# Optimization experiments

Hardware: AMD Instinct MI355X
Metric: run time of the kernel (lower is better)

## Reference

```python
import jax, jax.numpy as jnp
import numpy as np

N = 50000      # nodes
E = 800000     # edges
F_IN = 128     # input features
H = 128        # hidden width
C = 64         # classes


def _glorot(key, fan_in, fan_out):
    lim = float(np.sqrt(6.0 / (fan_in + fan_out)))
    return jax.random.uniform(key, (fan_in, fan_out), jnp.float32, -lim, lim)


def setup_inputs() -> dict:
    key = jax.random.key(0)
    ks = jax.random.split(key, 8)
    x = jax.random.normal(ks[0], (N, F_IN), jnp.float32)
    edge_index = jax.random.randint(ks[1], (2, E), 0, N, dtype=jnp.int64)
    return {
        "x": x,
        "edge_index": edge_index,
        "W0": _glorot(ks[2], F_IN, H), "b0": jnp.zeros((H,), jnp.float32),
        "W1": _glorot(ks[3], H, H),    "b1": jnp.zeros((H,), jnp.float32),
        "W2": _glorot(ks[4], H, C),    "b2": jnp.zeros((C,), jnp.float32),
    }


def _gcn_norm(edge_index, n):
    # add self-loops, then symmetric normalization D^-1/2 A D^-1/2
    loop = jnp.arange(n, dtype=edge_index.dtype)
    src = jnp.concatenate([edge_index[0], loop])   # message source j
    dst = jnp.concatenate([edge_index[1], loop])   # aggregation target i
    deg = jax.ops.segment_sum(jnp.ones_like(dst, jnp.float32), dst, num_segments=n)
    dinv = jnp.where(deg > 0, jax.lax.rsqrt(jnp.maximum(deg, 1.0)), 0.0)
    norm = dinv[src] * dinv[dst]                   # [E+N]
    return src, dst, norm


def _gcn_conv(x, W, b, src, dst, norm, n):
    h = x @ W                                      # [N, out]
    msg = norm[:, None] * h[src]                   # gather [E+N, out]
    out = jax.ops.segment_sum(msg, dst, num_segments=n)  # scatter-add
    return out + b


def reference(x, edge_index, W0, b0, W1, b1, W2, b2):
    n = x.shape[0]
    src, dst, norm = _gcn_norm(edge_index, n)
    h = _gcn_conv(x, W0, b0, src, dst, norm, n)
    h = h * jax.nn.sigmoid(h)                      # swish
    h = _gcn_conv(h, W1, b1, src, dst, norm, n)
    h = h * jax.nn.sigmoid(h)
    h = _gcn_conv(h, W2, b2, src, dst, norm, n)
    return jax.nn.log_softmax(h, axis=1)
```

## Files before the change

kernel.cpp:

```cpp
#include <hip/hip_runtime.h>


#define NODES_PER_BUCKET 1024
#define MAX_BUCKETS 64
#define CVT_BLOCKS 160

typedef __attribute__((ext_vector_type(8))) short short8;
typedef __attribute__((ext_vector_type(4))) float f32x4;

__device__ inline unsigned bf16_rn(float x) {
    unsigned u = __float_as_uint(x);
    return (u + 0x7fffu + ((u >> 16) & 1u)) >> 16;
}
__device__ inline float bf_lo(unsigned u) { return __uint_as_float(u << 16); }
__device__ inline float bf_hi(unsigned u) { return __uint_as_float(u & 0xffff0000u); }

__global__ __launch_bounds__(256) void prep_k(const int* __restrict__ dst, int e,
                                              int* __restrict__ bcnt,
                                              const float* __restrict__ W0,
                                              const float* __restrict__ W1,
                                              const float* __restrict__ W2,
                                              unsigned short* __restrict__ Wt) {
    const int t = threadIdx.x;
    if (blockIdx.x < CVT_BLOCKS) {
        int id = blockIdx.x * 256 + t;
        const float* W;
        int out, loc;
        if (id < 16384)      { W = W0; out = 128; loc = id; }
        else if (id < 32768) { W = W1; out = 128; loc = id - 16384; }
        else                 { W = W2; out = 64;  loc = id - 32768; }
        int o = loc >> 7, k = loc & 127;
        Wt[id] = (unsigned short)bf16_rn(W[k * out + o]);
        return;
    }
    __shared__ int h[MAX_BUCKETS];
    if (t < MAX_BUCKETS) h[t] = 0;
    __syncthreads();
    const int i0 = (blockIdx.x - CVT_BLOCKS) * 4096;
#pragma unroll
    for (int k = 0; k < 16; ++k) {
        int i = i0 + t + k * 256;
        if (i < e) atomicAdd(&h[dst[i] >> 10], 1);
    }
    __syncthreads();
    if (t < MAX_BUCKETS && h[t]) atomicAdd(&bcnt[t], h[t]);
}

__global__ __launch_bounds__(512) void scatter_k(const int* __restrict__ src,
                                                 const int* __restrict__ dst,
                                                 int e,
                                                 const int* __restrict__ bcnt,
                                                 int* __restrict__ scur,
                                                 unsigned* __restrict__ pairs) {
    __shared__ int bbase_s[MAX_BUCKETS];
    __shared__ int cnt[MAX_BUCKETS];
    __shared__ int cur[MAX_BUCKETS];
    __shared__ int gb[MAX_BUCKETS];
    const int t = threadIdx.x;
    if (t < MAX_BUCKETS) {
        int v = bcnt[t];
        int x = v;
#pragma unroll
        for (int off = 1; off < 64; off <<= 1) {
            int y = __shfl_up(x, off);
            if ((t & 63) >= off) x += y;
        }
        bbase_s[t] = x - v;
        cnt[t] = 0;
    }
    __syncthreads();
    const int i0 = blockIdx.x * 8192;
    int d[16];
#pragma unroll
    for (int k = 0; k < 16; ++k) {
        int i = i0 + t + k * 512;
        d[k] = (i < e) ? dst[i] : -1;
        if (d[k] >= 0) atomicAdd(&cnt[d[k] >> 10], 1);
    }
    __syncthreads();
    if (t < MAX_BUCKETS) {
        gb[t] = cnt[t] ? bbase_s[t] + atomicAdd(&scur[t], cnt[t]) : 0;
        cur[t] = 0;
    }
    __syncthreads();
#pragma unroll
    for (int k = 0; k < 16; ++k) {
        int i = i0 + t + k * 512;
        if (d[k] >= 0) {
            int b = d[k] >> 10;
            int r = atomicAdd(&cur[b], 1);
            pairs[gb[b] + r] = ((unsigned)src[i] << 10) | ((unsigned)d[k] & 1023u);
        }
    }
}

__global__ __launch_bounds__(1024) void build_k(const unsigned* __restrict__ pairs,
                                                const int* __restrict__ bcnt,
                                                int n, int e,
                                                int* __restrict__ rp,
                                                float* __restrict__ dinv,
                                                int* __restrict__ col) {
    __shared__ int hist[1024];
    __shared__ int tsum[1024];
    __shared__ int sE[2];
    const int t = threadIdx.x;
    if (t < MAX_BUCKETS) {
        int v = bcnt[t];
        int x = v;
#pragma unroll
        for (int off = 1; off < 64; off <<= 1) {
            int y = __shfl_up(x, off);
            if ((t & 63) >= off) x += y;
        }
        if (t == blockIdx.x) { sE[0] = x - v; sE[1] = x; }
    }
    hist[t] = 0;
    __syncthreads();
    const int ebase = sE[0];
    const int eend = sE[1];
    for (int i = ebase + t; i < eend; i += 1024)
        atomicAdd(&hist[pairs[i] & 1023u], 1);
    __syncthreads();
    const int deg = hist[t];
    tsum[t] = deg;
    __syncthreads();
    for (int off = 1; off < 1024; off <<= 1) {
        int x = (t >= off) ? tsum[t - off] : 0;
        __syncthreads();
        tsum[t] += x;
        __syncthreads();
    }
    const int excl = tsum[t] - deg;
    const int node0 = blockIdx.x << 10;
    if (node0 + t < n) {
        rp[node0 + t] = ebase + excl;
        dinv[node0 + t] = rsqrtf((float)(deg + 1));
    }
    hist[t] = excl;
    __syncthreads();
    for (int i = ebase + t; i < eend; i += 1024) {
        unsigned p = pairs[i];
        int r = atomicAdd(&hist[p & 1023u], 1);
        col[ebase + r] = (int)(p >> 10);
    }
    if (blockIdx.x == 0 && t == 0) rp[n] = e;
}

__global__ __launch_bounds__(256) void mfma_gemm0_k(
    const float* __restrict__ Af,
    const unsigned short* __restrict__ Wt,
    const float* __restrict__ dinv,
    unsigned short* __restrict__ G,
    int n) {
    __shared__ unsigned short lds[256 * 128];
    unsigned short* As = lds;
    unsigned short* Ws = lds + 128 * 128;

    const int tid = threadIdx.x;
    const int row0 = blockIdx.x * 128;

#pragma unroll
    for (int p = 0; p < 8; ++p) {
        int id = p * 256 + tid;
        int r = id >> 4, c = id & 15;
        uint4 v = make_uint4(0, 0, 0, 0);
        if (row0 + r < n) {
            const float4* fp = (const float4*)&Af[(size_t)(row0 + r) * 128 + c * 8];
            float4 v0 = fp[0], v1 = fp[1];
            v.x = bf16_rn(v0.x) | (bf16_rn(v0.y) << 16);
            v.y = bf16_rn(v0.z) | (bf16_rn(v0.w) << 16);
            v.z = bf16_rn(v1.x) | (bf16_rn(v1.y) << 16);
            v.w = bf16_rn(v1.z) | (bf16_rn(v1.w) << 16);
        }
        int bo = r * 256 + ((c * 16) ^ ((r & 7) << 4));
        *(uint4*)((char*)As + bo) = v;
    }
#pragma unroll
    for (int p = 0; p < 8; ++p) {
        int id = p * 256 + tid;
        int r = id >> 4, c = id & 15;
        uint4 v = *(const uint4*)&Wt[(size_t)r * 128 + c * 8];
        int bo = r * 256 + ((c * 16) ^ ((r & 7) << 4));
        *(uint4*)((char*)Ws + bo) = v;
    }
    __syncthreads();

    const int wid = tid >> 6, lane = tid & 63;
    const int lq = lane >> 4, lr = lane & 15;
    const int woff = wid * 32;

    f32x4 acc[2][8] = {};
#pragma unroll
    for (int ks = 0; ks < 4; ++ks) {
        short8 a[2];
#pragma unroll
        for (int m = 0; m < 2; ++m) {
            int r = woff + m * 16 + lr;
            int bo = r * 256 + ((lq * 16 + ks * 64) ^ ((r & 7) << 4));
            a[m] = *(const short8*)((const char*)As + bo);
        }
#pragma unroll
        for (int nf = 0; nf < 8; ++nf) {
            int c = nf * 16 + lr;
            int bo = c * 256 + ((lq * 16 + ks * 64) ^ ((c & 7) << 4));
            short8 b = *(const short8*)((const char*)Ws + bo);
            acc[0][nf] = __builtin_amdgcn_mfma_f32_16x16x32_bf16(a[0], b, acc[0][nf], 0, 0, 0);
            acc[1][nf] = __builtin_amdgcn_mfma_f32_16x16x32_bf16(a[1], b, acc[1][nf], 0, 0, 0);
        }
    }

#pragma unroll
    for (int m = 0; m < 2; ++m) {
#pragma unroll
        for (int j = 0; j < 4; ++j) {
            int r = row0 + woff + m * 16 + lq * 4 + j;
            if (r < n) {
                float d = dinv[r];
#pragma unroll
                for (int nf = 0; nf < 8; ++nf)
                    G[(size_t)r * 128 + nf * 16 + lr] =
                        (unsigned short)bf16_rn(d * acc[m][nf][j]);
            }
        }
    }
}

__device__ inline void acc8(float* a, uint4 u) {
    a[0] += bf_lo(u.x); a[1] += bf_hi(u.x);
    a[2] += bf_lo(u.y); a[3] += bf_hi(u.y);
    a[4] += bf_lo(u.z); a[5] += bf_hi(u.z);
    a[6] += bf_lo(u.w); a[7] += bf_hi(u.w);
}

template <int OUT>
__global__ __launch_bounds__(256, 4) void agg_gemm_k(
    const uint4* __restrict__ G4,
    const int* __restrict__ rp,
    const int* __restrict__ col,
    const float* __restrict__ dinv,
    const float* __restrict__ bias,
    const unsigned short* __restrict__ Wt,
    unsigned short* __restrict__ Gn,
    int n) {
    constexpr int NF = OUT / 16;
    __shared__ unsigned short lds[(64 + OUT) * 128];
    unsigned short* As = lds;
    unsigned short* Ws = lds + 64 * 128;

    const int tid = threadIdx.x;
    const int base = blockIdx.x * 64;
    const int sl = tid & 15;

    const float4 bl = *(const float4*)&bias[sl * 8];
    const float4 bh = *(const float4*)&bias[sl * 8 + 4];
#pragma unroll
    for (int q = 0; q < 4; ++q) {
        const int local = (tid >> 4) + q * 16;
        const int i = base + local;
        uint4 o = make_uint4(0, 0, 0, 0);
        if (i < n) {
            float a[8] = {0.f, 0.f, 0.f, 0.f, 0.f, 0.f, 0.f, 0.f};
            acc8(a, G4[(size_t)i * 16 + sl]);
            const int s = rp[i], e = rp[i + 1];
            int p = s;
            for (; p + 8 <= e; p += 8) {
                uint4 v[8];
#pragma unroll
                for (int k = 0; k < 8; ++k) {
                    int j = col[p + k];
                    v[k] = G4[(size_t)j * 16 + sl];
                }
#pragma unroll
                for (int k = 0; k < 8; ++k) acc8(a, v[k]);
            }
            if (p < e) {
                const int m = e - p;
                uint4 v[8];
#pragma unroll
                for (int k = 0; k < 8; ++k) {
                    int j = col[min(p + k, e - 1)];
                    v[k] = G4[(size_t)j * 16 + sl];
                }
#pragma unroll
                for (int k = 0; k < 8; ++k)
                    if (k < m) acc8(a, v[k]);
            }
            const float d = dinv[i];
            float r[8];
            r[0] = d * a[0] + bl.x; r[1] = d * a[1] + bl.y;
            r[2] = d * a[2] + bl.z; r[3] = d * a[3] + bl.w;
            r[4] = d * a[4] + bh.x; r[5] = d * a[5] + bh.y;
            r[6] = d * a[6] + bh.z; r[7] = d * a[7] + bh.w;
#pragma unroll
            for (int k = 0; k < 8; ++k) r[k] = r[k] / (1.f + expf(-r[k]));
            o.x = bf16_rn(r[0]) | (bf16_rn(r[1]) << 16);
            o.y = bf16_rn(r[2]) | (bf16_rn(r[3]) << 16);
            o.z = bf16_rn(r[4]) | (bf16_rn(r[5]) << 16);
            o.w = bf16_rn(r[6]) | (bf16_rn(r[7]) << 16);
        }
        int bo = local * 256 + ((sl * 16) ^ ((local & 7) << 4));
        *(uint4*)((char*)As + bo) = o;
    }

#pragma unroll
    for (int p = 0; p < OUT / 16; ++p) {
        int id = p * 256 + tid;
        int r = id >> 4, c = id & 15;
        uint4 v = *(const uint4*)&Wt[(size_t)r * 128 + c * 8];
        int bo = r * 256 + ((c * 16) ^ ((r & 7) << 4));
        *(uint4*)((char*)Ws + bo) = v;
    }
    __syncthreads();

    const int wid = tid >> 6, lane = tid & 63;
    const int lq = lane >> 4, lr = lane & 15;
    const int woff = wid * 16;

    f32x4 acc[NF] = {};
#pragma unroll
    for (int ks = 0; ks < 4; ++ks) {
        int r = woff + lr;
        int bo = r * 256 + ((lq * 16 + ks * 64) ^ ((r & 7) << 4));
        short8 a = *(const short8*)((const char*)As + bo);
#pragma unroll
        for (int nf = 0; nf < NF; ++nf) {
            int c = nf * 16 + lr;
            int wo = c * 256 + ((lq * 16 + ks * 64) ^ ((c & 7) << 4));
            short8 b = *(const short8*)((const char*)Ws + wo);
            acc[nf] = __builtin_amdgcn_mfma_f32_16x16x32_bf16(a, b, acc[nf], 0, 0, 0);
        }
    }

#pragma unroll
    for (int j = 0; j < 4; ++j) {
        int r = base + woff + lq * 4 + j;
        if (r < n) {
            float d = dinv[r];
#pragma unroll
            for (int nf = 0; nf < NF; ++nf)
                Gn[(size_t)r * OUT + nf * 16 + lr] =
                    (unsigned short)bf16_rn(d * acc[nf][j]);
        }
    }
}

__global__ __launch_bounds__(512, 4) void agg_lsm_k(const uint2* __restrict__ G2,
                                                    const int* __restrict__ rp,
                                                    const int* __restrict__ col,
                                                    const float* __restrict__ dinv,
                                                    const float* __restrict__ bias,
                                                    float* __restrict__ out, int n) {
    const int i = (blockIdx.x * blockDim.x + threadIdx.x) >> 4;
    const int sl = threadIdx.x & 15;
    if (i >= n) return;

    float a[4] = {0.f, 0.f, 0.f, 0.f};
    {
        uint2 u = G2[(size_t)i * 16 + sl];
        a[0] += bf_lo(u.x); a[1] += bf_hi(u.x);
        a[2] += bf_lo(u.y); a[3] += bf_hi(u.y);
    }
    const int s = rp[i], e = rp[i + 1];
    int p = s;
    for (; p + 8 <= e; p += 8) {
        uint2 v[8];
#pragma unroll
        for (int k = 0; k < 8; ++k) {
            int j = col[p + k];
            v[k] = G2[(size_t)j * 16 + sl];
        }
#pragma unroll
        for (int k = 0; k < 8; ++k) {
            a[0] += bf_lo(v[k].x); a[1] += bf_hi(v[k].x);
            a[2] += bf_lo(v[k].y); a[3] += bf_hi(v[k].y);
        }
    }
    if (p < e) {
        const int m = e - p;
        uint2 v[8];
#pragma unroll
        for (int k = 0; k < 8; ++k) {
            int j = col[min(p + k, e - 1)];
            v[k] = G2[(size_t)j * 16 + sl];
        }
#pragma unroll
        for (int k = 0; k < 8; ++k)
            if (k < m) {
                a[0] += bf_lo(v[k].x); a[1] += bf_hi(v[k].x);
                a[2] += bf_lo(v[k].y); a[3] += bf_hi(v[k].y);
            }
    }

    const float d = dinv[i];
    const float4 bv = *(const float4*)&bias[sl * 4];
    float lg[4];
    lg[0] = d * a[0] + bv.x; lg[1] = d * a[1] + bv.y;
    lg[2] = d * a[2] + bv.z; lg[3] = d * a[3] + bv.w;

    float m0 = fmaxf(fmaxf(lg[0], lg[1]), fmaxf(lg[2], lg[3]));
#pragma unroll
    for (int off = 1; off < 16; off <<= 1) m0 = fmaxf(m0, __shfl_xor(m0, off));
    float es = expf(lg[0] - m0) + expf(lg[1] - m0) +
               expf(lg[2] - m0) + expf(lg[3] - m0);
#pragma unroll
    for (int off = 1; off < 16; off <<= 1) es += __shfl_xor(es, off);
    const float lse = m0 + logf(es);
    float4 o;
    o.x = lg[0] - lse; o.y = lg[1] - lse; o.z = lg[2] - lse; o.w = lg[3] - lse;
    *(float4*)&out[(size_t)i * 64 + sl * 4] = o;
}

extern "C" void kernel_launch(void* const* d_in, const int* in_sizes, int n_in,
                              void* d_out, int out_size, void* d_ws, size_t ws_size,
                              hipStream_t stream) {
    const float* x = (const float*)d_in[0];
    const int* ei = (const int*)d_in[1];
    const float* W0 = (const float*)d_in[2];
    const float* b0 = (const float*)d_in[3];
    const float* W1 = (const float*)d_in[4];
    const float* b1 = (const float*)d_in[5];
    const float* W2 = (const float*)d_in[6];
    const float* b2 = (const float*)d_in[7];
    float* out = (float*)d_out;

    const int n = in_sizes[0] / 128;
    const int e = in_sizes[1] / 2;
    const int* src = ei;
    const int* dst = ei + e;

    char* ws = (char*)d_ws;
    size_t off = 0;
    auto alloc = [&](size_t bytes) -> void* {
        void* p = ws + off;
        off += (bytes + 255) & ~(size_t)255;
        return p;
    };
    int* bcnt = (int*)alloc(MAX_BUCKETS * 4 * 2);
    int* scur = bcnt + MAX_BUCKETS;
    int* rp = (int*)alloc((size_t)(n + 1) * 4);
    float* dinv = (float*)alloc((size_t)n * 4);
    int* col = (int*)alloc((size_t)e * 4);
    unsigned* pairs = (unsigned*)alloc((size_t)e * 4);
    unsigned short* wt = (unsigned short*)alloc(40960 * 2);
    unsigned short* ga = (unsigned short*)alloc((size_t)n * 256);
    unsigned short* gb = (unsigned short*)alloc((size_t)n * 256);

    unsigned short* w0t = wt;
    unsigned short* w1t = wt + 16384;
    unsigned short* w2t = wt + 32768;

    hipMemsetAsync(bcnt, 0, MAX_BUCKETS * 4 * 2, stream);
    prep_k<<<CVT_BLOCKS + (e + 4095) / 4096, 256, 0, stream>>>(dst, e, bcnt,
                                                               W0, W1, W2, wt);
    scatter_k<<<(e + 8191) / 8192, 512, 0, stream>>>(src, dst, e, bcnt, scur, pairs);
    const int nbuck = (n + NODES_PER_BUCKET - 1) / NODES_PER_BUCKET;
    build_k<<<nbuck, 1024, 0, stream>>>(pairs, bcnt, n, e, rp, dinv, col);

    const int gb128 = (n + 127) / 128;
    const int fb = (n + 63) / 64;
    const int ab = (n + 31) / 32;

    mfma_gemm0_k<<<gb128, 256, 0, stream>>>(x, w0t, dinv, ga, n);
    agg_gemm_k<128><<<fb, 256, 0, stream>>>((const uint4*)ga, rp, col, dinv, b0,
                                            w1t, gb, n);
    agg_gemm_k<64><<<fb, 256, 0, stream>>>((const uint4*)gb, rp, col, dinv, b1,
                                           w2t, ga, n);
    agg_lsm_k<<<ab, 512, 0, stream>>>((const uint2*)ga, rp, col, dinv, b2, out, n);
}
```

Before: 162.5 us.

## Shrink fused agg-GEMM tile to 32 rows and read weights directly from global

The fused aggregation+GEMM kernel now handles 32 nodes per block instead of 64. The four waves are split into two row strips times two output-column halves. The weight tile is no longer staged in LDS; each wave loads its B fragments straight from global memory, where the weights should stay cache-resident. This cuts LDS use and per-block staging cost, raising occupancy and block count for the latency-bound gather. In exchange, each block re-reads weights from global/L2, and there are twice as many blocks.

```diff
diff --git a/kernel.cpp b/kernel.cpp
--- a/kernel.cpp
+++ b/kernel.cpp
@@ -242,19 +242,18 @@
     const unsigned short* __restrict__ Wt,
     unsigned short* __restrict__ Gn,
     int n) {
-    constexpr int NF = OUT / 16;
-    __shared__ unsigned short lds[(64 + OUT) * 128];
-    unsigned short* As = lds;
-    unsigned short* Ws = lds + 64 * 128;
+    constexpr int HC = OUT / 2;
+    constexpr int NF = OUT / 32;
+    __shared__ unsigned short As[32 * 128];
 
     const int tid = threadIdx.x;
-    const int base = blockIdx.x * 64;
+    const int base = blockIdx.x * 32;
     const int sl = tid & 15;
 
     const float4 bl = *(const float4*)&bias[sl * 8];
     const float4 bh = *(const float4*)&bias[sl * 8 + 4];
 #pragma unroll
-    for (int q = 0; q < 4; ++q) {
+    for (int q = 0; q < 2; ++q) {
         const int local = (tid >> 4) + q * 16;
         const int i = base + local;
         uint4 o = make_uint4(0, 0, 0, 0);
@@ -301,44 +300,35 @@
         int bo = local * 256 + ((sl * 16) ^ ((local & 7) << 4));
         *(uint4*)((char*)As + bo) = o;
     }
-
-#pragma unroll
-    for (int p = 0; p < OUT / 16; ++p) {
-        int id = p * 256 + tid;
-        int r = id >> 4, c = id & 15;
-        uint4 v = *(const uint4*)&Wt[(size_t)r * 128 + c * 8];
-        int bo = r * 256 + ((c * 16) ^ ((r & 7) << 4));
-        *(uint4*)((char*)Ws + bo) = v;
-    }
     __syncthreads();
 
     const int wid = tid >> 6, lane = tid & 63;
     const int lq = lane >> 4, lr = lane & 15;
-    const int woff = wid * 16;
+    const int strip = wid >> 1;
+    const int half = wid & 1;
 
     f32x4 acc[NF] = {};
 #pragma unroll
     for (int ks = 0; ks < 4; ++ks) {
-        int r = woff + lr;
+        int r = strip * 16 + lr;
         int bo = r * 256 + ((lq * 16 + ks * 64) ^ ((r & 7) << 4));
         short8 a = *(const short8*)((const char*)As + bo);
 #pragma unroll
         for (int nf = 0; nf < NF; ++nf) {
-            int c = nf * 16 + lr;
-            int wo = c * 256 + ((lq * 16 + ks * 64) ^ ((c & 7) << 4));
-            short8 b = *(const short8*)((const char*)Ws + wo);
+            int c = half * HC + nf * 16 + lr;
+            short8 b = *(const short8*)&Wt[(size_t)c * 128 + ks * 32 + lq * 8];
             acc[nf] = __builtin_amdgcn_mfma_f32_16x16x32_bf16(a, b, acc[nf], 0, 0, 0);
         }
     }
 
 #pragma unroll
     for (int j = 0; j < 4; ++j) {
-        int r = base + woff + lq * 4 + j;
+        int r = base + strip * 16 + lq * 4 + j;
         if (r < n) {
             float d = dinv[r];
 #pragma unroll
             for (int nf = 0; nf < NF; ++nf)
-                Gn[(size_t)r * OUT + nf * 16 + lr] =
+                Gn[(size_t)r * OUT + half * HC + nf * 16 + lr] =
                     (unsigned short)bf16_rn(d * acc[nf][j]);
         }
     }
@@ -443,7 +433,7 @@
     unsigned* pairs = (unsigned*)alloc((size_t)e * 4);
     unsigned short* wt = (unsigned short*)alloc(40960 * 2);
     unsigned short* ga = (unsigned short*)alloc((size_t)n * 256);
-    unsigned short* gb = (unsigned short*)alloc((size_t)n * 256);
+    unsigned short* gbuf = (unsigned short*)alloc((size_t)n * 256);
 
     unsigned short* w0t = wt;
     unsigned short* w1t = wt + 16384;
@@ -457,13 +447,13 @@
     build_k<<<nbuck, 1024, 0, stream>>>(pairs, bcnt, n, e, rp, dinv, col);
 
     const int gb128 = (n + 127) / 128;
-    const int fb = (n + 63) / 64;
+    const int fb = (n + 31) / 32;
     const int ab = (n + 31) / 32;
 
     mfma_gemm0_k<<<gb128, 256, 0, stream>>>(x, w0t, dinv, ga, n);
     agg_gemm_k<128><<<fb, 256, 0, stream>>>((const uint4*)ga, rp, col, dinv, b0,
-                                            w1t, gb, n);
-    agg_gemm_k<64><<<fb, 256, 0, stream>>>((const uint4*)gb, rp, col, dinv, b1,
+                                            w1t, gbuf, n);
+    agg_gemm_k<64><<<fb, 256, 0, stream>>>((const uint4*)gbuf, rp, col, dinv, b1,
                                            w2t, ga, n);
     agg_lsm_k<<<ab, 512, 0, stream>>>((const uint2*)ga, rp, col, dinv, b2, out, n);
 }
```

Measured after the change: 164.7 us. Within noise of the previous version (+1.4%).
